# Performance work log

Hardware: AMD Instinct MI355X
Metric: run time of the kernel (lower is better)

## Reference

```python
import jax, jax.numpy as jnp
import numpy as np

B, QL, L = 4, 1024, 2048          # batch, new query tokens, cache capacity
H, KVH, D = 16, 4, 128            # query heads, kv heads (GQA), head dim
G = H // KVH                      # query heads per kv head
SCALE = 1.0 / float(np.sqrt(D))
NEG = jnp.float32(-1e30)


def setup_inputs() -> dict:
    key = jax.random.key(0)
    ks = jax.random.split(key, 6)
    return {
        "q": jax.random.normal(ks[0], (B, QL, H * D), jnp.float32),
        "k": jax.random.normal(ks[1], (B, QL, KVH * D), jnp.float32),
        "v": jax.random.normal(ks[2], (B, QL, KVH * D), jnp.float32),
        "cache_k": jax.random.normal(ks[3], (B, KVH, L, D), jnp.float32),
        "cache_v": jax.random.normal(ks[4], (B, KVH, L, D), jnp.float32),
        "seq_lens": jax.random.randint(ks[5], (B,), 0, L - QL, jnp.int32),
    }


def reference(q, k, v, cache_k, cache_v, seq_lens):
    bs, ql, _ = q.shape
    # split heads; scale applied to q as in _jax_attn_func
    qh = (q.reshape(bs, ql, H, D) * SCALE).swapaxes(1, 2)   # [B,H,QL,D]
    kh = k.reshape(bs, ql, KVH, D)                           # [B,QL,KVH,D]
    vh = v.reshape(bs, ql, KVH, D)
    # write new tokens into the kv cache at per-sequence positions (ragged)
    pos = seq_lens[:, None] + jnp.arange(ql)                 # [B,QL]
    bidx = jnp.arange(bs)[:, None]                           # [B,1]
    new_ck = cache_k.at[bidx, :, pos].set(kh)                # [B,KVH,L,D]
    new_cv = cache_v.at[bidx, :, pos].set(vh)
    # GQA attention over the full cache with ragged-causal mask
    qg = qh.reshape(bs, KVH, G, ql, D)                       # [B,KVH,G,QL,D]
    scores = jnp.einsum('bkgqd,bkld->bkgql', qg, new_ck)     # [B,KVH,G,QL,L]
    limit = seq_lens[:, None, None, None, None] + jnp.arange(ql)[None, None, None, :, None]
    valid = jnp.arange(L)[None, None, None, None, :] <= limit
    scores = jnp.where(valid, scores, NEG)
    probs = jax.nn.softmax(scores, axis=-1)
    outg = jnp.einsum('bkgql,bkld->bkgqd', probs, new_cv)    # [B,KVH,G,QL,D]
    out = outg.reshape(bs, H, ql, D).swapaxes(1, 2).reshape(bs, ql, H * D)
    return (out, new_ck, new_cv)
```

## Files before the change

kernel.cpp:

```cpp
#include <hip/hip_runtime.h>
#include <hip/hip_bf16.h>
#include <stdint.h>

#define NB 4
#define NQL 1024
#define NL 2048
#define NH 16
#define NKVH 4
#define ND 128
#define KVBLK 64
#define QSCALE_LOG2E 0.1275174340213733f

typedef __bf16 bf16_t;
typedef __bf16 bf16x4 __attribute__((ext_vector_type(4)));
typedef __bf16 bf16x8 __attribute__((ext_vector_type(8)));
typedef float f32x4 __attribute__((ext_vector_type(4)));
typedef float f32x16 __attribute__((ext_vector_type(16)));
typedef uint32_t u32;
typedef unsigned short u16;

__device__ __forceinline__ void gload_lds16(const void* g, void* l) {
  __builtin_amdgcn_global_load_lds((const __attribute__((address_space(1))) void*)g,
                                   (__attribute__((address_space(3))) void*)l,
                                   16, 0, 0);
}

__device__ __forceinline__ u32 pack_bf16(float a, float b) {
  u32 ua = (u32)__builtin_bit_cast(u16, (bf16_t)a);
  u32 ub = (u32)__builtin_bit_cast(u16, (bf16_t)b);
  return ua | (ub << 16);
}

__global__ __launch_bounds__(256) void update_cache_kernel(
    const float* __restrict__ knew,
    const float* __restrict__ vnew,
    const float* __restrict__ cache_k,
    const float* __restrict__ cache_v,
    const int*   __restrict__ seq_lens,
    float* __restrict__ new_ck,
    float* __restrict__ new_cv,
    bf16_t* __restrict__ kb)
{
  const int n4 = NB * NKVH * NL * ND / 4;
  for (int i = blockIdx.x * blockDim.x + threadIdx.x; i < 2 * n4;
       i += gridDim.x * blockDim.x) {
    const int which = i >= n4;
    const int j   = which ? i - n4 : i;
    const int d4  = j & 31;
    const int l   = (j >> 5) & (NL - 1);
    const int kvh = (j >> 16) & (NKVH - 1);
    const int b   = j >> 18;
    const int s   = seq_lens[b];
    float4 val;
    if (l >= s && l < s + NQL) {
      const float* nsrc = which ? vnew : knew;
      val = *(const float4*)(nsrc + (((size_t)(b * NQL + (l - s))) * NKVH + kvh) * ND + d4 * 4);
    } else {
      const float* csrc = which ? cache_v : cache_k;
      val = *(const float4*)(csrc + (((size_t)(b * NKVH + kvh)) * NL + l) * ND + d4 * 4);
    }
    const size_t coff = (((size_t)(b * NKVH + kvh)) * NL + l) * ND + d4 * 4;
    float* dst = which ? new_cv : new_ck;
    *(float4*)(dst + coff) = val;
    if (!which) {
      bf16x4 kv;
      kv[0] = (bf16_t)val.x; kv[1] = (bf16_t)val.y;
      kv[2] = (bf16_t)val.z; kv[3] = (bf16_t)val.w;
      *(bf16x4*)(kb + coff) = kv;
    }
  }
}

__global__ __launch_bounds__(256) void transpose_v_kernel(
    const float* __restrict__ new_cv, bf16_t* __restrict__ vt)
{
  __shared__ float T[64][129];
  const int tid = threadIdx.x;
  const int bid = blockIdx.x;
  const int lt  = bid & 31;
  const int kvh = (bid >> 5) & (NKVH - 1);
  const int b   = bid >> 7;
  const int l0  = lt * 64;

  const float* src = new_cv + (((size_t)(b * NKVH + kvh)) * NL + l0) * ND;
  #pragma unroll
  for (int j = 0; j < 8; ++j) {
    const int i   = tid + j * 256;
    const int row = i >> 5, c4 = i & 31;
    float4 v = *(const float4*)(src + row * ND + c4 * 4);
    T[row][c4 * 4 + 0] = v.x; T[row][c4 * 4 + 1] = v.y;
    T[row][c4 * 4 + 2] = v.z; T[row][c4 * 4 + 3] = v.w;
  }
  __syncthreads();
  bf16_t* dst = vt + ((size_t)(b * NKVH + kvh)) * ND * NL;
  #pragma unroll
  for (int j = 0; j < 4; ++j) {
    const int c = tid + j * 256;
    const int d = c >> 3, l8 = c & 7;
    bf16x8 o;
    #pragma unroll
    for (int e = 0; e < 8; ++e) o[e] = (bf16_t)T[l8 * 8 + e][d];
    *(bf16x8*)(dst + (size_t)d * NL + l0 + l8 * 8) = o;
  }
}

#define STAGE(buf, tt) do {                                                  \
    const int l0s = (tt) * KVBLK;                                            \
    _Pragma("unroll")                                                        \
    for (int j = 0; j < 4; ++j) {                                            \
      const int ck = tid + j * 256;                                          \
      const int kr = ck >> 4, kc2 = (ck & 15) ^ (kr & 7);                    \
      gload_lds16(kbb + (size_t)(l0s + kr) * ND + kc2 * 8,                   \
                  &Kl[buf][(wave * 64 + j * 256) * 8]);                      \
      const int vr = ck >> 3, vc2 = (ck & 7) ^ (vr & 7);                     \
      gload_lds16(vtb + (size_t)vr * NL + (l0s + vc2 * 8),                   \
                  &Vl[buf][(wave * 64 + j * 256) * 8]);                      \
    }                                                                        \
  } while (0)

__global__ __launch_bounds__(256, 2) void attn_kernel(
    const float* __restrict__ qin, const bf16_t* __restrict__ kb,
    const bf16_t* __restrict__ vt, const int* __restrict__ seq_lens,
    float* __restrict__ out)
{
  __shared__ bf16_t Kl[2][KVBLK * ND];
  __shared__ bf16_t Vl[2][ND * KVBLK];

  const int tid  = threadIdx.x;
  const int wave = tid >> 6, lane = tid & 63;
  const int l5   = lane & 31;
  const int hi5  = lane >> 5;

  const int bid  = blockIdx.x;
  const int half = bid >> 8, r = bid & 255;
  const int b    = r >> 6;
  const int h    = (r >> 2) & (NH - 1);
  const int qt   = half ? (7 - ((r & 3) << 1)) : ((r & 3) << 1);
  const int kvh  = h >> 2;
  const int s    = seq_lens[b];
  const int qw   = qt * 128 + wave * 32;
  const int q    = qw + l5;

  const bf16_t* kbb = kb + ((size_t)(b * NKVH + kvh)) * NL * ND;
  const bf16_t* vtb = vt + ((size_t)(b * NKVH + kvh)) * ND * NL;

  bf16x8 qf[8];
  {
    const float* qb = qin + ((size_t)((b * NQL + q) * NH + h)) * ND;
    #pragma unroll
    for (int kc = 0; kc < 8; ++kc) {
      float4 x0 = *(const float4*)(qb + kc * 16 + hi5 * 8);
      float4 x1 = *(const float4*)(qb + kc * 16 + hi5 * 8 + 4);
      bf16x8 f;
      f[0] = (bf16_t)(x0.x * QSCALE_LOG2E); f[1] = (bf16_t)(x0.y * QSCALE_LOG2E);
      f[2] = (bf16_t)(x0.z * QSCALE_LOG2E); f[3] = (bf16_t)(x0.w * QSCALE_LOG2E);
      f[4] = (bf16_t)(x1.x * QSCALE_LOG2E); f[5] = (bf16_t)(x1.y * QSCALE_LOG2E);
      f[6] = (bf16_t)(x1.z * QSCALE_LOG2E); f[7] = (bf16_t)(x1.w * QSCALE_LOG2E);
      qf[kc] = f;
    }
  }

  f32x16 oacc[4];
  #pragma unroll
  for (int i = 0; i < 4; ++i) oacc[i] = (f32x16)(0.f);
  float mreg = -1e30f, lreg = 0.f;

  const int ntiles = (s + qt * 128 + 128 + KVBLK - 1) / KVBLK;
  int cur = 0;
  STAGE(0, 0);
  __syncthreads();

  for (int t = 0; t < ntiles; ++t) {
    const int l0 = t * KVBLK;
    if (t + 1 < ntiles) STAGE(cur ^ 1, t + 1);

    if (l0 <= s + qw + 31) {
      f32x16 sacc[2];
      #pragma unroll
      for (int sl = 0; sl < 2; ++sl) {
        f32x16 acc = (f32x16)(0.f);
        const int krow = sl * 32 + l5;
        #pragma unroll
        for (int kc = 0; kc < 8; ++kc) {
          bf16x8 kf = *(const bf16x8*)
              &Kl[cur][krow * ND + (((kc * 2 + hi5) ^ (l5 & 7)) * 8)];
          acc = __builtin_amdgcn_mfma_f32_32x32x16_bf16(kf, qf[kc], acc, 0, 0, 0);
        }
        sacc[sl] = acc;
      }
      if (l0 + 63 > s + qw) {
        const int lim = s + q - l0;
        #pragma unroll
        for (int sl = 0; sl < 2; ++sl)
          #pragma unroll
          for (int rr = 0; rr < 16; ++rr) {
            const int ll = sl * 32 + (rr & 3) + 8 * (rr >> 2) + 4 * hi5;
            if (ll > lim) sacc[sl][rr] = -1e30f;
          }
      }
      float pmax = sacc[0][0];
      #pragma unroll
      for (int sl = 0; sl < 2; ++sl)
        #pragma unroll
        for (int rr = 0; rr < 16; ++rr) pmax = fmaxf(pmax, sacc[sl][rr]);
      pmax = fmaxf(pmax, __shfl_xor(pmax, 32, 64));
      if (!__all(pmax - mreg <= 8.f)) {
        const float mnew  = fmaxf(mreg, pmax);
        const float alpha = exp2f(mreg - mnew);
        mreg = mnew;
        lreg *= alpha;
        #pragma unroll
        for (int i = 0; i < 4; ++i) oacc[i] *= alpha;
      }
      float tsum = 0.f;
      #pragma unroll
      for (int sl = 0; sl < 2; ++sl)
        #pragma unroll
        for (int rr = 0; rr < 16; ++rr) {
          const float p = exp2f(sacc[sl][rr] - mreg);
          sacc[sl][rr] = p;
          tsum += p;
        }
      lreg += tsum + __shfl_xor(tsum, 32, 64);

      u32 pk[2][4][2];
      #pragma unroll
      for (int sl = 0; sl < 2; ++sl)
        #pragma unroll
        for (int m = 0; m < 4; ++m) {
          pk[sl][m][0] = pack_bf16(sacc[sl][m * 4 + 0], sacc[sl][m * 4 + 1]);
          pk[sl][m][1] = pack_bf16(sacc[sl][m * 4 + 2], sacc[sl][m * 4 + 3]);
        }
      bf16x8 pb[4];
      #pragma unroll
      for (int c = 0; c < 4; ++c) {
        const int slp = c >> 1;
        const u32 k0 = hi5 ? pk[slp][(2 * c + 1) & 3][0] : pk[slp][(2 * c) & 3][0];
        const u32 k1 = hi5 ? pk[slp][(2 * c + 1) & 3][1] : pk[slp][(2 * c) & 3][1];
        const u32 s0 = hi5 ? pk[slp][(2 * c) & 3][0] : pk[slp][(2 * c + 1) & 3][0];
        const u32 s1 = hi5 ? pk[slp][(2 * c) & 3][1] : pk[slp][(2 * c + 1) & 3][1];
        const u32 r0 = (u32)__shfl_xor((int)s0, 32, 64);
        const u32 r1 = (u32)__shfl_xor((int)s1, 32, 64);
        union { u32 w[4]; bf16x8 v; } u;
        u.w[0] = hi5 ? r0 : k0;
        u.w[1] = hi5 ? r1 : k1;
        u.w[2] = hi5 ? k0 : r0;
        u.w[3] = hi5 ? k1 : r1;
        pb[c] = u.v;
      }
      #pragma unroll
      for (int ds = 0; ds < 4; ++ds) {
        const int vrow = ds * 32 + l5;
        #pragma unroll
        for (int c = 0; c < 4; ++c) {
          bf16x8 va = *(const bf16x8*)
              &Vl[cur][vrow * KVBLK + (((c * 2 + hi5) ^ (l5 & 7)) * 8)];
          oacc[ds] = __builtin_amdgcn_mfma_f32_32x32x16_bf16(va, pb[c], oacc[ds], 0, 0, 0);
        }
      }
    }
    __syncthreads();
    cur ^= 1;
  }

  const float linv = 1.0f / lreg;
  float* ob = out + ((size_t)((b * NQL + q) * NH + h)) * ND;
  #pragma unroll
  for (int ds = 0; ds < 4; ++ds)
    #pragma unroll
    for (int rq = 0; rq < 4; ++rq) {
      float4 v;
      v.x = oacc[ds][rq * 4 + 0] * linv;
      v.y = oacc[ds][rq * 4 + 1] * linv;
      v.z = oacc[ds][rq * 4 + 2] * linv;
      v.w = oacc[ds][rq * 4 + 3] * linv;
      *(float4*)(ob + ds * 32 + rq * 8 + hi5 * 4) = v;
    }
}

extern "C" void kernel_launch(void* const* d_in, const int* in_sizes, int n_in,
                              void* d_out, int out_size, void* d_ws, size_t ws_size,
                              hipStream_t stream)
{
  const float* q        = (const float*)d_in[0];
  const float* k        = (const float*)d_in[1];
  const float* v        = (const float*)d_in[2];
  const float* cache_k  = (const float*)d_in[3];
  const float* cache_v  = (const float*)d_in[4];
  const int*   seq_lens = (const int*)d_in[5];

  float* out    = (float*)d_out;
  float* new_ck = out + (size_t)NB * NQL * NH * ND;
  float* new_cv = new_ck + (size_t)NB * NKVH * NL * ND;

  bf16_t* kb = (bf16_t*)d_ws;
  bf16_t* vt = kb + (size_t)NB * NKVH * NL * ND;

  hipLaunchKernelGGL(update_cache_kernel, dim3(2048), dim3(256), 0, stream,
                     k, v, cache_k, cache_v, seq_lens, new_ck, new_cv, kb);
  hipLaunchKernelGGL(transpose_v_kernel, dim3(NB * NKVH * (NL / 64)), dim3(256), 0, stream,
                     new_cv, vt);
  hipLaunchKernelGGL(attn_kernel, dim3(512), dim3(256), 0, stream,
                     q, kb, vt, seq_lens, out);
}
```

Measured before the change: 106.7 us.

## Software-pipeline QK^T of the next KV tile with softmax and PV of current

Splits K and V staging into separate macros and restructures the KV loop into a two-tile ping-pong. The QK^T MFMAs for tile t+1 are issued before the softmax and PV for tile t, and K is prefetched two tiles ahead while V is prefetched one ahead. The goal is to overlap the matrix work with the softmax math and the global-to-LDS loads, so MFMA units idle less between dependent phases. In exchange, a second live score accumulator raises register pressure, and the unrolled loop body roughly doubles code size.

Result: slower. 110.2 us (+3.2%).

```diff
diff --git a/kernel.cpp b/kernel.cpp
--- a/kernel.cpp
+++ b/kernel.cpp
@@ -104,7 +104,7 @@
   }
 }
 
-#define STAGE(buf, tt) do {                                                  \
+#define STAGE_K(buf, tt) do {                                                \
     const int l0s = (tt) * KVBLK;                                            \
     _Pragma("unroll")                                                        \
     for (int j = 0; j < 4; ++j) {                                            \
@@ -112,9 +112,104 @@
       const int kr = ck >> 4, kc2 = (ck & 15) ^ (kr & 7);                    \
       gload_lds16(kbb + (size_t)(l0s + kr) * ND + kc2 * 8,                   \
                   &Kl[buf][(wave * 64 + j * 256) * 8]);                      \
+    }                                                                        \
+  } while (0)
+
+#define STAGE_V(buf, tt) do {                                                \
+    const int l0s = (tt) * KVBLK;                                            \
+    _Pragma("unroll")                                                        \
+    for (int j = 0; j < 4; ++j) {                                            \
+      const int ck = tid + j * 256;                                          \
       const int vr = ck >> 3, vc2 = (ck & 7) ^ (vr & 7);                     \
       gload_lds16(vtb + (size_t)vr * NL + (l0s + vc2 * 8),                   \
                   &Vl[buf][(wave * 64 + j * 256) * 8]);                      \
+    }                                                                        \
+  } while (0)
+
+#define QKT(SB, KBI) do {                                                    \
+    _Pragma("unroll")                                                        \
+    for (int sl = 0; sl < 2; ++sl) {                                         \
+      f32x16 acc = (f32x16)(0.f);                                            \
+      const int krow = sl * 32 + l5;                                         \
+      _Pragma("unroll")                                                      \
+      for (int kc = 0; kc < 8; ++kc) {                                       \
+        bf16x8 kf = *(const bf16x8*)                                         \
+            &Kl[KBI][krow * ND + (((kc * 2 + hi5) ^ (l5 & 7)) * 8)];         \
+        acc = __builtin_amdgcn_mfma_f32_32x32x16_bf16(kf, qf[kc], acc, 0, 0, 0); \
+      }                                                                      \
+      SB[sl] = acc;                                                          \
+    }                                                                        \
+  } while (0)
+
+#define SOFTPV(SB, VBI, L0) do {                                             \
+    if ((L0) + 63 > s + qw) {                                                \
+      const int lim = s + q - (L0);                                          \
+      _Pragma("unroll")                                                      \
+      for (int sl = 0; sl < 2; ++sl)                                         \
+        _Pragma("unroll")                                                    \
+        for (int rr = 0; rr < 16; ++rr) {                                    \
+          const int ll = sl * 32 + (rr & 3) + 8 * (rr >> 2) + 4 * hi5;       \
+          if (ll > lim) SB[sl][rr] = -1e30f;                                 \
+        }                                                                    \
+    }                                                                        \
+    float pmax = SB[0][0];                                                   \
+    _Pragma("unroll")                                                        \
+    for (int sl = 0; sl < 2; ++sl)                                           \
+      _Pragma("unroll")                                                      \
+      for (int rr = 0; rr < 16; ++rr) pmax = fmaxf(pmax, SB[sl][rr]);        \
+    pmax = fmaxf(pmax, __shfl_xor(pmax, 32, 64));                            \
+    if (!__all(pmax - mreg <= 8.f)) {                                        \
+      const float mnew  = fmaxf(mreg, pmax);                                 \
+      const float alpha = exp2f(mreg - mnew);                                \
+      mreg = mnew;                                                           \
+      lreg *= alpha;                                                         \
+      _Pragma("unroll")                                                      \
+      for (int i = 0; i < 4; ++i) oacc[i] *= alpha;                          \
+    }                                                                        \
+    float tsum = 0.f;                                                        \
+    _Pragma("unroll")                                                        \
+    for (int sl = 0; sl < 2; ++sl)                                           \
+      _Pragma("unroll")                                                      \
+      for (int rr = 0; rr < 16; ++rr) {                                      \
+        const float p = exp2f(SB[sl][rr] - mreg);                            \
+        SB[sl][rr] = p;                                                      \
+        tsum += p;                                                           \
+      }                                                                      \
+    lreg += tsum + __shfl_xor(tsum, 32, 64);                                 \
+    u32 pk[2][4][2];                                                         \
+    _Pragma("unroll")                                                        \
+    for (int sl = 0; sl < 2; ++sl)                                           \
+      _Pragma("unroll")                                                      \
+      for (int m = 0; m < 4; ++m) {                                          \
+        pk[sl][m][0] = pack_bf16(SB[sl][m * 4 + 0], SB[sl][m * 4 + 1]);      \
+        pk[sl][m][1] = pack_bf16(SB[sl][m * 4 + 2], SB[sl][m * 4 + 3]);      \
+      }                                                                      \
+    bf16x8 pb[4];                                                            \
+    _Pragma("unroll")                                                        \
+    for (int c = 0; c < 4; ++c) {                                            \
+      const int slp = c >> 1;                                                \
+      const u32 k0 = hi5 ? pk[slp][(2 * c + 1) & 3][0] : pk[slp][(2 * c) & 3][0]; \
+      const u32 k1 = hi5 ? pk[slp][(2 * c + 1) & 3][1] : pk[slp][(2 * c) & 3][1]; \
+      const u32 s0 = hi5 ? pk[slp][(2 * c) & 3][0] : pk[slp][(2 * c + 1) & 3][0]; \
+      const u32 s1 = hi5 ? pk[slp][(2 * c) & 3][1] : pk[slp][(2 * c + 1) & 3][1]; \
+      const u32 r0 = (u32)__shfl_xor((int)s0, 32, 64);                       \
+      const u32 r1 = (u32)__shfl_xor((int)s1, 32, 64);                       \
+      union { u32 w[4]; bf16x8 v; } u;                                       \
+      u.w[0] = hi5 ? r0 : k0;                                                \
+      u.w[1] = hi5 ? r1 : k1;                                                \
+      u.w[2] = hi5 ? k0 : r0;                                                \
+      u.w[3] = hi5 ? k1 : r1;                                                \
+      pb[c] = u.v;                                                           \
+    }                                                                        \
+    _Pragma("unroll")                                                        \
+    for (int ds = 0; ds < 4; ++ds) {                                         \
+      const int vrow = ds * 32 + l5;                                         \
+      _Pragma("unroll")                                                      \
+      for (int c = 0; c < 4; ++c) {                                          \
+        bf16x8 va = *(const bf16x8*)                                         \
+            &Vl[VBI][vrow * KVBLK + (((c * 2 + hi5) ^ (l5 & 7)) * 8)];       \
+        oacc[ds] = __builtin_amdgcn_mfma_f32_32x32x16_bf16(va, pb[c], oacc[ds], 0, 0, 0); \
+      }                                                                      \
     }                                                                        \
   } while (0)
 
@@ -166,101 +261,31 @@
   float mreg = -1e30f, lreg = 0.f;
 
   const int ntiles = (s + qt * 128 + 128 + KVBLK - 1) / KVBLK;
-  int cur = 0;
-  STAGE(0, 0);
+
+  STAGE_K(0, 0);
+  STAGE_V(0, 0);
+  STAGE_K(1, 1);
   __syncthreads();
 
-  for (int t = 0; t < ntiles; ++t) {
-    const int l0 = t * KVBLK;
-    if (t + 1 < ntiles) STAGE(cur ^ 1, t + 1);
-
-    if (l0 <= s + qw + 31) {
-      f32x16 sacc[2];
-      #pragma unroll
-      for (int sl = 0; sl < 2; ++sl) {
-        f32x16 acc = (f32x16)(0.f);
-        const int krow = sl * 32 + l5;
-        #pragma unroll
-        for (int kc = 0; kc < 8; ++kc) {
-          bf16x8 kf = *(const bf16x8*)
-              &Kl[cur][krow * ND + (((kc * 2 + hi5) ^ (l5 & 7)) * 8)];
-          acc = __builtin_amdgcn_mfma_f32_32x32x16_bf16(kf, qf[kc], acc, 0, 0, 0);
-        }
-        sacc[sl] = acc;
-      }
-      if (l0 + 63 > s + qw) {
-        const int lim = s + q - l0;
-        #pragma unroll
-        for (int sl = 0; sl < 2; ++sl)
-          #pragma unroll
-          for (int rr = 0; rr < 16; ++rr) {
-            const int ll = sl * 32 + (rr & 3) + 8 * (rr >> 2) + 4 * hi5;
-            if (ll > lim) sacc[sl][rr] = -1e30f;
-          }
-      }
-      float pmax = sacc[0][0];
-      #pragma unroll
-      for (int sl = 0; sl < 2; ++sl)
-        #pragma unroll
-        for (int rr = 0; rr < 16; ++rr) pmax = fmaxf(pmax, sacc[sl][rr]);
-      pmax = fmaxf(pmax, __shfl_xor(pmax, 32, 64));
-      if (!__all(pmax - mreg <= 8.f)) {
-        const float mnew  = fmaxf(mreg, pmax);
-        const float alpha = exp2f(mreg - mnew);
-        mreg = mnew;
-        lreg *= alpha;
-        #pragma unroll
-        for (int i = 0; i < 4; ++i) oacc[i] *= alpha;
-      }
-      float tsum = 0.f;
-      #pragma unroll
-      for (int sl = 0; sl < 2; ++sl)
-        #pragma unroll
-        for (int rr = 0; rr < 16; ++rr) {
-          const float p = exp2f(sacc[sl][rr] - mreg);
-          sacc[sl][rr] = p;
-          tsum += p;
-        }
-      lreg += tsum + __shfl_xor(tsum, 32, 64);
-
-      u32 pk[2][4][2];
-      #pragma unroll
-      for (int sl = 0; sl < 2; ++sl)
-        #pragma unroll
-        for (int m = 0; m < 4; ++m) {
-          pk[sl][m][0] = pack_bf16(sacc[sl][m * 4 + 0], sacc[sl][m * 4 + 1]);
-          pk[sl][m][1] = pack_bf16(sacc[sl][m * 4 + 2], sacc[sl][m * 4 + 3]);
-        }
-      bf16x8 pb[4];
-      #pragma unroll
-      for (int c = 0; c < 4; ++c) {
-        const int slp = c >> 1;
-        const u32 k0 = hi5 ? pk[slp][(2 * c + 1) & 3][0] : pk[slp][(2 * c) & 3][0];
-        const u32 k1 = hi5 ? pk[slp][(2 * c + 1) & 3][1] : pk[slp][(2 * c) & 3][1];
-        const u32 s0 = hi5 ? pk[slp][(2 * c) & 3][0] : pk[slp][(2 * c + 1) & 3][0];
-        const u32 s1 = hi5 ? pk[slp][(2 * c) & 3][1] : pk[slp][(2 * c + 1) & 3][1];
-        const u32 r0 = (u32)__shfl_xor((int)s0, 32, 64);
-        const u32 r1 = (u32)__shfl_xor((int)s1, 32, 64);
-        union { u32 w[4]; bf16x8 v; } u;
-        u.w[0] = hi5 ? r0 : k0;
-        u.w[1] = hi5 ? r1 : k1;
-        u.w[2] = hi5 ? k0 : r0;
-        u.w[3] = hi5 ? k1 : r1;
-        pb[c] = u.v;
-      }
-      #pragma unroll
-      for (int ds = 0; ds < 4; ++ds) {
-        const int vrow = ds * 32 + l5;
-        #pragma unroll
-        for (int c = 0; c < 4; ++c) {
-          bf16x8 va = *(const bf16x8*)
-              &Vl[cur][vrow * KVBLK + (((c * 2 + hi5) ^ (l5 & 7)) * 8)];
-          oacc[ds] = __builtin_amdgcn_mfma_f32_32x32x16_bf16(va, pb[c], oacc[ds], 0, 0, 0);
-        }
-      }
-    }
+  f32x16 sA[2], sB[2];
+  QKT(sA, 0);
+
+  for (int t = 0; ; t += 2) {
     __syncthreads();
-    cur ^= 1;
+    if (t + 2 < ntiles) STAGE_K(0, t + 2);
+    if (t + 1 < ntiles) STAGE_V(1, t + 1);
+    const bool gB = (t + 1 < ntiles) && ((t + 1) * KVBLK <= s + qw + 31);
+    if (gB) QKT(sB, 1);
+    if (t * KVBLK <= s + qw + 31) SOFTPV(sA, 0, t * KVBLK);
+    if (t + 1 >= ntiles) break;
+
+    __syncthreads();
+    if (t + 3 < ntiles) STAGE_K(1, t + 3);
+    if (t + 2 < ntiles) STAGE_V(0, t + 2);
+    const bool gA = (t + 2 < ntiles) && ((t + 2) * KVBLK <= s + qw + 31);
+    if (gA) QKT(sA, 0);
+    if ((t + 1) * KVBLK <= s + qw + 31) SOFTPV(sB, 1, (t + 1) * KVBLK);
+    if (t + 2 >= ntiles) break;
   }
 
   const float linv = 1.0f / lreg;
```
